# Performance work log

Hardware: AMD Instinct MI355X
Metric: run time of the kernel (lower is better)

Reference implementation:

```python
import jax, jax.numpy as jnp
import numpy as np

EMBED_DIM = 1024

def setup_inputs() -> dict:
    key = jax.random.key(0)
    kx, kq, kk, kv = jax.random.split(key, 4)
    scale = 1.0 / np.sqrt(EMBED_DIM)  # Kaiming-uniform-ish init scale
    x = jax.random.normal(kx, (4, 2048, EMBED_DIM), dtype=jnp.float32)
    Wq = jax.random.uniform(kq, (EMBED_DIM, EMBED_DIM), jnp.float32, -scale, scale)
    Wk = jax.random.uniform(kk, (EMBED_DIM, EMBED_DIM), jnp.float32, -scale, scale)
    Wv = jax.random.uniform(kv, (EMBED_DIM, EMBED_DIM), jnp.float32, -scale, scale)
    return {"x": x, "Wq": Wq, "Wk": Wk, "Wv": Wv}

def reference(x, Wq, Wk, Wv):
    # Linear layers: y = x @ W.T (torch nn.Linear convention, no bias)
    q = jnp.einsum('bsd,ed->bse', x, Wq)
    k = jnp.einsum('bsd,ed->bse', x, Wk)
    v = jnp.einsum('bsd,ed->bse', x, Wv)
    d = k.shape[-1]
    scores = jnp.einsum('bqe,bke->bqk', q, k) / jnp.sqrt(jnp.asarray(d, x.dtype))
    attn = jax.nn.softmax(scores, axis=-1)
    return jnp.einsum('bqk,bke->bqe', attn, v)
```

## Files before the change

### kernel.cpp

```cpp
#include <hip/hip_runtime.h>
#include <hip/hip_bf16.h>

typedef unsigned short u16;
typedef __bf16 bf16x8 __attribute__((ext_vector_type(8)));
typedef float f32x4 __attribute__((ext_vector_type(4)));

#define MEMF() asm volatile("" ::: "memory")

__device__ __forceinline__ u16 f2bf(float f) {
    unsigned int u = __builtin_bit_cast(unsigned int, f);
    unsigned int r = u + 0x7FFFu + ((u >> 16) & 1u);
    return (u16)(r >> 16);
}

__device__ __forceinline__ float bf2f(unsigned int bits16) {
    return __builtin_bit_cast(float, bits16 << 16);
}

__device__ __forceinline__ void gload_lds16(const u16* g, u16* l) {
    __builtin_amdgcn_global_load_lds(
        (const __attribute__((address_space(1))) void*)(g),
        (__attribute__((address_space(3))) void*)(l), 16, 0, 0);
}

__global__ __launch_bounds__(256) void cvt_bf16_kernel(
    const float* __restrict__ in, u16* __restrict__ out, int n8)
{
    int i = blockIdx.x * 256 + threadIdx.x;
    if (i >= n8) return;
    const float4* p = (const float4*)in + 2 * (long long)i;
    float4 a = p[0], b = p[1];
    uint4 o;
    o.x = (unsigned)f2bf(a.x) | ((unsigned)f2bf(a.y) << 16);
    o.y = (unsigned)f2bf(a.z) | ((unsigned)f2bf(a.w) << 16);
    o.z = (unsigned)f2bf(b.x) | ((unsigned)f2bf(b.y) << 16);
    o.w = (unsigned)f2bf(b.z) | ((unsigned)f2bf(b.w) << 16);
    ((uint4*)out)[i] = o;
}

template <int BN, bool OUT_F32>
__global__ __launch_bounds__(512, 2) void gemm4p(
    const u16* __restrict__ A, const u16* __restrict__ B, void* __restrict__ Cv,
    int lda, int ldb, int ldc, int K,
    long long sAz, long long sBz, long long sCz, int cw, int ch)
{
    constexpr int WC = (BN == 256) ? 4 : 2;
    constexpr int ROWS = (BN == 256) ? 128 : 64;
    constexpr int MI = ROWS / 16;
    constexpr int MIh = MI / 2;
    constexpr int BLOADS = BN / 64;
    constexpr int BNK = BN * 64;

    extern __shared__ u16 lds[];
    u16* ldsB = lds + 32768;

    const int flat = blockIdx.x + gridDim.x * blockIdx.y;
    const int xcd = flat & 7, jj = flat >> 3;
    const int nCx = gridDim.x / cw;
    const int bx = (xcd % nCx) * cw + jj % cw;
    const int by = (xcd / nCx) * ch + jj / cw;

    const int z = blockIdx.z;
    A += (long long)z * sAz;
    B += (long long)z * sBz;

    const int tid  = threadIdx.x;
    const int lane = tid & 63;
    const int wave = tid >> 6;
    const int wr = wave / WC, wc = wave % WC;
    const int m0 = by << 8, n0 = bx * BN;
    const int NT = K >> 6;

    const u16* gAp[4];
    const u16* gBp[BLOADS];
#pragma unroll
    for (int i = 0; i < 4; ++i) {
        int s = tid + i * 512, row = ((s >> 7) << 4) | (s & 15), g = (s >> 4) & 7;
        gAp[i] = A + (long long)(m0 + row) * lda + g * 8;
    }
#pragma unroll
    for (int i = 0; i < BLOADS; ++i) {
        int s = tid + i * 512, row = ((s >> 7) << 4) | (s & 15), g = (s >> 4) & 7;
        gBp[i] = B + (long long)(n0 + row) * ldb + g * 8;
    }
    auto stA = [&](int kt, int buf, int i) {
        gload_lds16(gAp[i] + (long long)kt * 64, lds + buf * 16384 + (tid + i * 512) * 8);
    };
    auto stB = [&](int kt, int buf, int i) {
        gload_lds16(gBp[i] + (long long)kt * 64, ldsB + buf * BNK + (tid + i * 512) * 8);
    };

    f32x4 acc[MI][4] = {};

#pragma unroll
    for (int i = 0; i < 4; ++i) stA(0, 0, i);
#pragma unroll
    for (int i = 0; i < BLOADS; ++i) stB(0, 0, i);
#pragma unroll
    for (int i = 0; i < 4; ++i) stA(1, 1, i);
#pragma unroll
    for (int i = 0; i < BLOADS; ++i) stB(1, 1, i);
    if constexpr (BN == 256) asm volatile("s_waitcnt vmcnt(8)" ::: "memory");
    else                     asm volatile("s_waitcnt vmcnt(6)" ::: "memory");
    __builtin_amdgcn_s_barrier();
    MEMF();

    for (int kt = 0; kt < NT; ++kt) {
        const int cur = kt & 1;
        const u16* sAc = lds  + cur * 16384 + lane * 8;
        const u16* sBc = ldsB + cur * BNK   + lane * 8;
        const bool st = (kt + 2 < NT);

        bf16x8 a[MIh][2], b0[2][2], b1[2][2];

#pragma unroll
        for (int mi = 0; mi < MIh; ++mi)
#pragma unroll
            for (int kk = 0; kk < 2; ++kk)
                a[mi][kk] = *(const bf16x8*)(sAc + ((wr * MI + mi) * 8 + kk * 4) * 128);
#pragma unroll
        for (int ni = 0; ni < 2; ++ni)
#pragma unroll
            for (int kk = 0; kk < 2; ++kk)
                b0[ni][kk] = *(const bf16x8*)(sBc + ((wc * 4 + ni) * 8 + kk * 4) * 128);
        MEMF(); __builtin_amdgcn_s_barrier();
        asm volatile("s_waitcnt lgkmcnt(0)" ::: "memory");
        __builtin_amdgcn_s_setprio(1);
#pragma unroll
        for (int kk = 0; kk < 2; ++kk)
#pragma unroll
            for (int mi = 0; mi < MIh; ++mi)
#pragma unroll
                for (int ni = 0; ni < 2; ++ni)
                    acc[mi][ni] = __builtin_amdgcn_mfma_f32_16x16x32_bf16(
                        a[mi][kk], b0[ni][kk], acc[mi][ni], 0, 0, 0);
        __builtin_amdgcn_s_setprio(0);
        MEMF(); __builtin_amdgcn_s_barrier();

#pragma unroll
        for (int ni = 0; ni < 2; ++ni)
#pragma unroll
            for (int kk = 0; kk < 2; ++kk)
                b1[ni][kk] = *(const bf16x8*)(sBc + ((wc * 4 + 2 + ni) * 8 + kk * 4) * 128);
        if constexpr (BN == 256) {
            if (st) { stA(kt + 2, cur, 0); stA(kt + 2, cur, 2); }
        }
        MEMF(); __builtin_amdgcn_s_barrier();
        asm volatile("s_waitcnt lgkmcnt(0)" ::: "memory");
        __builtin_amdgcn_s_setprio(1);
#pragma unroll
        for (int kk = 0; kk < 2; ++kk)
#pragma unroll
            for (int mi = 0; mi < MIh; ++mi)
#pragma unroll
                for (int ni = 0; ni < 2; ++ni)
                    acc[mi][2 + ni] = __builtin_amdgcn_mfma_f32_16x16x32_bf16(
                        a[mi][kk], b1[ni][kk], acc[mi][2 + ni], 0, 0, 0);
        __builtin_amdgcn_s_setprio(0);
        MEMF(); __builtin_amdgcn_s_barrier();

#pragma unroll
        for (int mi = 0; mi < MIh; ++mi)
#pragma unroll
            for (int kk = 0; kk < 2; ++kk)
                a[mi][kk] = *(const bf16x8*)(sAc + ((wr * MI + MIh + mi) * 8 + kk * 4) * 128);
        if (st) {
            if constexpr (BN == 256) { stB(kt + 2, cur, 0); stB(kt + 2, cur, 1); }
            else                     { stB(kt + 2, cur, 0); }
        }
        MEMF(); __builtin_amdgcn_s_barrier();
        asm volatile("s_waitcnt lgkmcnt(0)" ::: "memory");
        __builtin_amdgcn_s_setprio(1);
#pragma unroll
        for (int kk = 0; kk < 2; ++kk)
#pragma unroll
            for (int mi = 0; mi < MIh; ++mi)
#pragma unroll
                for (int ni = 0; ni < 2; ++ni)
                    acc[MIh + mi][ni] = __builtin_amdgcn_mfma_f32_16x16x32_bf16(
                        a[mi][kk], b0[ni][kk], acc[MIh + mi][ni], 0, 0, 0);
        __builtin_amdgcn_s_setprio(0);
        MEMF(); __builtin_amdgcn_s_barrier();

        if (st) {
            if constexpr (BN == 256) {
                stA(kt + 2, cur, 1); stA(kt + 2, cur, 3);
                stB(kt + 2, cur, 2); stB(kt + 2, cur, 3);
            } else {
                stA(kt + 2, cur, 0); stA(kt + 2, cur, 1);
                stA(kt + 2, cur, 2); stA(kt + 2, cur, 3);
                stB(kt + 2, cur, 1);
            }
        }
        MEMF(); __builtin_amdgcn_s_barrier();
        __builtin_amdgcn_s_setprio(1);
#pragma unroll
        for (int kk = 0; kk < 2; ++kk)
#pragma unroll
            for (int mi = 0; mi < MIh; ++mi)
#pragma unroll
                for (int ni = 0; ni < 2; ++ni)
                    acc[MIh + mi][2 + ni] = __builtin_amdgcn_mfma_f32_16x16x32_bf16(
                        a[mi][kk], b1[ni][kk], acc[MIh + mi][2 + ni], 0, 0, 0);
        __builtin_amdgcn_s_setprio(0);
        if (st) {
            if constexpr (BN == 256) asm volatile("s_waitcnt vmcnt(8)" ::: "memory");
            else                     asm volatile("s_waitcnt vmcnt(6)" ::: "memory");
        } else if (kt + 1 < NT) {
            asm volatile("s_waitcnt vmcnt(0)" ::: "memory");
        }
        MEMF(); __builtin_amdgcn_s_barrier();
    }

    const int fl = lane & 15, fg = lane >> 4;
    const int er0 = m0 + wr * ROWS + fg * 4;
    const int ec0 = n0 + wc * 64 + fl;
    if constexpr (OUT_F32) {
        float* C = (float*)Cv + (long long)z * sCz;
#pragma unroll
        for (int mi = 0; mi < MI; ++mi)
#pragma unroll
            for (int ni = 0; ni < 4; ++ni)
#pragma unroll
                for (int j = 0; j < 4; ++j)
                    C[(long long)(er0 + mi * 16 + j) * ldc + ec0 + ni * 16] = acc[mi][ni][j];
    } else {
        u16* C = (u16*)Cv + (long long)z * sCz;
#pragma unroll
        for (int mi = 0; mi < MI; ++mi)
#pragma unroll
            for (int ni = 0; ni < 4; ++ni)
#pragma unroll
                for (int j = 0; j < 4; ++j)
                    C[(long long)(er0 + mi * 16 + j) * ldc + ec0 + ni * 16] = f2bf(acc[mi][ni][j]);
    }
}

__global__ __launch_bounds__(256) void softmax_rows(u16* __restrict__ S)
{
    const long long row = blockIdx.x;
    u16* p = S + row * 2048;
    const int tid = threadIdx.x;
    const int lane = tid & 63, wave = tid >> 6;

    uint4 r4 = ((const uint4*)p)[tid];
    unsigned u[4] = {r4.x, r4.y, r4.z, r4.w};
    float v[8];
    const float scale = 1.0f / 32.0f;
#pragma unroll
    for (int i = 0; i < 4; ++i) {
        v[2 * i]     = bf2f(u[i] & 0xFFFFu) * scale;
        v[2 * i + 1] = __builtin_bit_cast(float, u[i] & 0xFFFF0000u) * scale;
    }
    float mx = v[0];
#pragma unroll
    for (int i = 1; i < 8; ++i) mx = fmaxf(mx, v[i]);
#pragma unroll
    for (int off = 32; off >= 1; off >>= 1) mx = fmaxf(mx, __shfl_xor(mx, off, 64));

    __shared__ float redmax[4], redsum[4];
    if (lane == 0) redmax[wave] = mx;
    __syncthreads();
    mx = fmaxf(fmaxf(redmax[0], redmax[1]), fmaxf(redmax[2], redmax[3]));

    float s = 0.f;
#pragma unroll
    for (int i = 0; i < 8; ++i) { v[i] = __expf(v[i] - mx); s += v[i]; }
#pragma unroll
    for (int off = 32; off >= 1; off >>= 1) s += __shfl_xor(s, off, 64);
    if (lane == 0) redsum[wave] = s;
    __syncthreads();
    s = redsum[0] + redsum[1] + redsum[2] + redsum[3];
    float inv = 1.0f / s;

    uint4 o;
    unsigned ov[4];
#pragma unroll
    for (int i = 0; i < 4; ++i)
        ov[i] = (unsigned)f2bf(v[2 * i] * inv) |
                ((unsigned)f2bf(v[2 * i + 1] * inv) << 16);
    o.x = ov[0]; o.y = ov[1]; o.z = ov[2]; o.w = ov[3];
    ((uint4*)p)[tid] = o;
}

extern "C" void kernel_launch(void* const* d_in, const int* in_sizes, int n_in,
                              void* d_out, int out_size, void* d_ws, size_t ws_size,
                              hipStream_t stream) {
    const float* x  = (const float*)d_in[0];
    const float* Wq = (const float*)d_in[1];
    const float* Wk = (const float*)d_in[2];
    const float* Wv = (const float*)d_in[3];
    float* out = (float*)d_out;

    const int B = 4, S = 2048, D = 1024;
    const long long MS = (long long)B * S;

    u16* Sc  = (u16*)d_ws;
    u16* xb  = Sc;
    u16* wqk = Sc  + (long long)B * S * S;
    u16* wvb = wqk + 2 * D * D;
    u16* qk  = wvb + D * D;
    u16* vT  = qk  + MS * 2 * D;
    size_t need = (size_t)2 * ((long long)B * S * S + 3 * D * D + MS * 2 * D + MS * D);
    if (ws_size < need) return;

    hipFuncSetAttribute(reinterpret_cast<const void*>(&gemm4p<256, false>),
                        hipFuncAttributeMaxDynamicSharedMemorySize, 131072);
    hipFuncSetAttribute(reinterpret_cast<const void*>(&gemm4p<128, false>),
                        hipFuncAttributeMaxDynamicSharedMemorySize, 98304);
    hipFuncSetAttribute(reinterpret_cast<const void*>(&gemm4p<128, true>),
                        hipFuncAttributeMaxDynamicSharedMemorySize, 98304);

    cvt_bf16_kernel<<<(int)(MS * D / 8 / 256), 256, 0, stream>>>(x, xb, (int)(MS * D / 8));
    cvt_bf16_kernel<<<D * D / 8 / 256, 256, 0, stream>>>(Wq, wqk, D * D / 8);
    cvt_bf16_kernel<<<D * D / 8 / 256, 256, 0, stream>>>(Wk, wqk + D * D, D * D / 8);
    cvt_bf16_kernel<<<D * D / 8 / 256, 256, 0, stream>>>(Wv, wvb, D * D / 8);

    gemm4p<256, false><<<dim3(2 * D / 256, (int)(MS / 256), 1), 512, 131072, stream>>>(
        xb, wqk, qk, D, D, 2 * D, D, 0, 0, 0, 8, 4);

    gemm4p<128, false><<<dim3((int)(MS / 128), D / 256, 1), 512, 98304, stream>>>(
        wvb, xb, vT, D, D, (int)MS, D, 0, 0, 0, 8, 4);

    gemm4p<256, false><<<dim3(S / 256, S / 256, B), 512, 131072, stream>>>(
        qk, qk + D, Sc, 2 * D, 2 * D, S, D,
        (long long)S * 2 * D, (long long)S * 2 * D, (long long)S * S, 2, 4);

    softmax_rows<<<(int)(B * S), 256, 0, stream>>>(Sc);

    gemm4p<128, true><<<dim3(D / 128, S / 256, B), 512, 98304, stream>>>(
        Sc, vT, out, S, (int)MS, D, S,
        (long long)S * S, (long long)S, (long long)S * D, 4, 2);
}
```

Baseline: 195.3 us.

## Double-buffer MFMA fragments in registers and prefetch next k-tile during compute

Restructures the GEMM main loop so the next k-tile's A and B fragments are read from LDS into separate register sets (a0/a1, b0/b1) while MFMAs for the current tile run. Global-to-LDS staging for tile kt+2 is now issued in one batch instead of being spread across the four phases. Explicit lgkmcnt waits are replaced by sched_barriers so LDS reads can overlap with matrix math. The cost is more registers and a full vmcnt(0) drain each iteration. There is also a possible race: the next buffer is read right after the wait with no barrier, so other waves' LDS writes may not be visible yet.

```diff
diff --git a/kernel.cpp b/kernel.cpp
--- a/kernel.cpp
+++ b/kernel.cpp
@@ -4,8 +4,6 @@
 typedef unsigned short u16;
 typedef __bf16 bf16x8 __attribute__((ext_vector_type(8)));
 typedef float f32x4 __attribute__((ext_vector_type(4)));
-
-#define MEMF() asm volatile("" ::: "memory")
 
 __device__ __forceinline__ u16 f2bf(float f) {
     unsigned int u = __builtin_bit_cast(unsigned int, f);
@@ -83,48 +81,48 @@
         int s = tid + i * 512, row = ((s >> 7) << 4) | (s & 15), g = (s >> 4) & 7;
         gBp[i] = B + (long long)(n0 + row) * ldb + g * 8;
     }
-    auto stA = [&](int kt, int buf, int i) {
-        gload_lds16(gAp[i] + (long long)kt * 64, lds + buf * 16384 + (tid + i * 512) * 8);
+    auto stage = [&](int kt, int buf) {
+#pragma unroll
+        for (int i = 0; i < 4; ++i)
+            gload_lds16(gAp[i] + (long long)kt * 64, lds + buf * 16384 + (tid + i * 512) * 8);
+#pragma unroll
+        for (int i = 0; i < BLOADS; ++i)
+            gload_lds16(gBp[i] + (long long)kt * 64, ldsB + buf * BNK + (tid + i * 512) * 8);
     };
-    auto stB = [&](int kt, int buf, int i) {
-        gload_lds16(gBp[i] + (long long)kt * 64, ldsB + buf * BNK + (tid + i * 512) * 8);
-    };
 
     f32x4 acc[MI][4] = {};
-
-#pragma unroll
-    for (int i = 0; i < 4; ++i) stA(0, 0, i);
-#pragma unroll
-    for (int i = 0; i < BLOADS; ++i) stB(0, 0, i);
-#pragma unroll
-    for (int i = 0; i < 4; ++i) stA(1, 1, i);
-#pragma unroll
-    for (int i = 0; i < BLOADS; ++i) stB(1, 1, i);
+    bf16x8 a0[MIh][2], a1[MIh][2], b0[2][2], b1[2][2];
+
+    stage(0, 0);
+    stage(1, 1);
     if constexpr (BN == 256) asm volatile("s_waitcnt vmcnt(8)" ::: "memory");
     else                     asm volatile("s_waitcnt vmcnt(6)" ::: "memory");
     __builtin_amdgcn_s_barrier();
-    MEMF();
+#pragma unroll
+    for (int mi = 0; mi < MIh; ++mi)
+#pragma unroll
+        for (int kk = 0; kk < 2; ++kk)
+            a0[mi][kk] = *(const bf16x8*)(lds + lane * 8 + ((wr * MI + mi) * 8 + kk * 4) * 128);
+#pragma unroll
+    for (int ni = 0; ni < 2; ++ni)
+#pragma unroll
+        for (int kk = 0; kk < 2; ++kk)
+            b0[ni][kk] = *(const bf16x8*)(ldsB + lane * 8 + ((wc * 4 + ni) * 8 + kk * 4) * 128);
 
     for (int kt = 0; kt < NT; ++kt) {
         const int cur = kt & 1;
         const u16* sAc = lds  + cur * 16384 + lane * 8;
         const u16* sBc = ldsB + cur * BNK   + lane * 8;
-        const bool st = (kt + 2 < NT);
-
-        bf16x8 a[MIh][2], b0[2][2], b1[2][2];
-
-#pragma unroll
-        for (int mi = 0; mi < MIh; ++mi)
+        const u16* sAn = lds  + (cur ^ 1) * 16384 + lane * 8;
+        const u16* sBn = ldsB + (cur ^ 1) * BNK   + lane * 8;
+
+#pragma unroll
+        for (int ni = 0; ni < 2; ++ni)
 #pragma unroll
             for (int kk = 0; kk < 2; ++kk)
-                a[mi][kk] = *(const bf16x8*)(sAc + ((wr * MI + mi) * 8 + kk * 4) * 128);
-#pragma unroll
-        for (int ni = 0; ni < 2; ++ni)
-#pragma unroll
-            for (int kk = 0; kk < 2; ++kk)
-                b0[ni][kk] = *(const bf16x8*)(sBc + ((wc * 4 + ni) * 8 + kk * 4) * 128);
-        MEMF(); __builtin_amdgcn_s_barrier();
-        asm volatile("s_waitcnt lgkmcnt(0)" ::: "memory");
+                b1[ni][kk] = *(const bf16x8*)(sBc + ((wc * 4 + 2 + ni) * 8 + kk * 4) * 128);
+        __builtin_amdgcn_sched_barrier(0);
+        __builtin_amdgcn_s_barrier();
         __builtin_amdgcn_s_setprio(1);
 #pragma unroll
         for (int kk = 0; kk < 2; ++kk)
@@ -133,20 +131,17 @@
 #pragma unroll
                 for (int ni = 0; ni < 2; ++ni)
                     acc[mi][ni] = __builtin_amdgcn_mfma_f32_16x16x32_bf16(
-                        a[mi][kk], b0[ni][kk], acc[mi][ni], 0, 0, 0);
+                        a0[mi][kk], b0[ni][kk], acc[mi][ni], 0, 0, 0);
         __builtin_amdgcn_s_setprio(0);
-        MEMF(); __builtin_amdgcn_s_barrier();
-
-#pragma unroll
-        for (int ni = 0; ni < 2; ++ni)
+        __builtin_amdgcn_s_barrier();
+
+#pragma unroll
+        for (int mi = 0; mi < MIh; ++mi)
 #pragma unroll
             for (int kk = 0; kk < 2; ++kk)
-                b1[ni][kk] = *(const bf16x8*)(sBc + ((wc * 4 + 2 + ni) * 8 + kk * 4) * 128);
-        if constexpr (BN == 256) {
-            if (st) { stA(kt + 2, cur, 0); stA(kt + 2, cur, 2); }
-        }
-        MEMF(); __builtin_amdgcn_s_barrier();
-        asm volatile("s_waitcnt lgkmcnt(0)" ::: "memory");
+                a1[mi][kk] = *(const bf16x8*)(sAc + ((wr * MI + MIh + mi) * 8 + kk * 4) * 128);
+        __builtin_amdgcn_sched_barrier(0);
+        __builtin_amdgcn_s_barrier();
         __builtin_amdgcn_s_setprio(1);
 #pragma unroll
         for (int kk = 0; kk < 2; ++kk)
@@ -155,21 +150,20 @@
 #pragma unroll
                 for (int ni = 0; ni < 2; ++ni)
                     acc[mi][2 + ni] = __builtin_amdgcn_mfma_f32_16x16x32_bf16(
-                        a[mi][kk], b1[ni][kk], acc[mi][2 + ni], 0, 0, 0);
+                        a0[mi][kk], b1[ni][kk], acc[mi][2 + ni], 0, 0, 0);
         __builtin_amdgcn_s_setprio(0);
-        MEMF(); __builtin_amdgcn_s_barrier();
-
-#pragma unroll
-        for (int mi = 0; mi < MIh; ++mi)
-#pragma unroll
-            for (int kk = 0; kk < 2; ++kk)
-                a[mi][kk] = *(const bf16x8*)(sAc + ((wr * MI + MIh + mi) * 8 + kk * 4) * 128);
-        if (st) {
-            if constexpr (BN == 256) { stB(kt + 2, cur, 0); stB(kt + 2, cur, 1); }
-            else                     { stB(kt + 2, cur, 0); }
+        __builtin_amdgcn_s_barrier();
+
+        if (kt + 1 < NT) {
+            asm volatile("s_waitcnt vmcnt(0)" ::: "memory");
+#pragma unroll
+            for (int mi = 0; mi < MIh; ++mi)
+#pragma unroll
+                for (int kk = 0; kk < 2; ++kk)
+                    a0[mi][kk] = *(const bf16x8*)(sAn + ((wr * MI + mi) * 8 + kk * 4) * 128);
         }
-        MEMF(); __builtin_amdgcn_s_barrier();
-        asm volatile("s_waitcnt lgkmcnt(0)" ::: "memory");
+        __builtin_amdgcn_sched_barrier(0);
+        __builtin_amdgcn_s_barrier();
         __builtin_amdgcn_s_setprio(1);
 #pragma unroll
         for (int kk = 0; kk < 2; ++kk)
@@ -178,21 +172,20 @@
 #pragma unroll
                 for (int ni = 0; ni < 2; ++ni)
                     acc[MIh + mi][ni] = __builtin_amdgcn_mfma_f32_16x16x32_bf16(
-                        a[mi][kk], b0[ni][kk], acc[MIh + mi][ni], 0, 0, 0);
+                        a1[mi][kk], b0[ni][kk], acc[MIh + mi][ni], 0, 0, 0);
         __builtin_amdgcn_s_setprio(0);
-        MEMF(); __builtin_amdgcn_s_barrier();
-
-        if (st) {
-            if constexpr (BN == 256) {
-                stA(kt + 2, cur, 1); stA(kt + 2, cur, 3);
-                stB(kt + 2, cur, 2); stB(kt + 2, cur, 3);
-            } else {
-                stA(kt + 2, cur, 0); stA(kt + 2, cur, 1);
-                stA(kt + 2, cur, 2); stA(kt + 2, cur, 3);
-                stB(kt + 2, cur, 1);
-            }
+        __builtin_amdgcn_s_barrier();
+
+        if (kt + 2 < NT) stage(kt + 2, cur);
+        if (kt + 1 < NT) {
+#pragma unroll
+            for (int ni = 0; ni < 2; ++ni)
+#pragma unroll
+                for (int kk = 0; kk < 2; ++kk)
+                    b0[ni][kk] = *(const bf16x8*)(sBn + ((wc * 4 + ni) * 8 + kk * 4) * 128);
         }
-        MEMF(); __builtin_amdgcn_s_barrier();
+        __builtin_amdgcn_sched_barrier(0);
+        __builtin_amdgcn_s_barrier();
         __builtin_amdgcn_s_setprio(1);
 #pragma unroll
         for (int kk = 0; kk < 2; ++kk)
@@ -201,15 +194,9 @@
 #pragma unroll
                 for (int ni = 0; ni < 2; ++ni)
                     acc[MIh + mi][2 + ni] = __builtin_amdgcn_mfma_f32_16x16x32_bf16(
-                        a[mi][kk], b1[ni][kk], acc[MIh + mi][2 + ni], 0, 0, 0);
+                        a1[mi][kk], b1[ni][kk], acc[MIh + mi][2 + ni], 0, 0, 0);
         __builtin_amdgcn_s_setprio(0);
-        if (st) {
-            if constexpr (BN == 256) asm volatile("s_waitcnt vmcnt(8)" ::: "memory");
-            else                     asm volatile("s_waitcnt vmcnt(6)" ::: "memory");
-        } else if (kt + 1 < NT) {
-            asm volatile("s_waitcnt vmcnt(0)" ::: "memory");
-        }
-        MEMF(); __builtin_amdgcn_s_barrier();
+        __builtin_amdgcn_s_barrier();
     }
 
     const int fl = lane & 15, fg = lane >> 4;
```

Measured after the change: 227.2 us. +16.3%, slower.

## Fuse softmax into QK^T epilogue and defer normalization to PV epilogue

Applied to the files above, without the earlier changes.

Removes the standalone softmax pass. The QK^T GEMM epilogue now writes exp(score/32) directly as bf16 and emits per-tile row-sum partials. A small kernel reduces those partials to inverse sums, and the PV GEMM scales its output rows by them. The three weight conversions are merged into one launch, and the compiler memory fences around barriers are dropped. The change skips max subtraction, which is safe for these input scales but could overflow for larger scores, and removing the fences risks compiler reordering of LDS accesses.

```diff
diff --git a/kernel.cpp b/kernel.cpp
--- a/kernel.cpp
+++ b/kernel.cpp
@@ -4,8 +4,6 @@
 typedef unsigned short u16;
 typedef __bf16 bf16x8 __attribute__((ext_vector_type(8)));
 typedef float f32x4 __attribute__((ext_vector_type(4)));
-
-#define MEMF() asm volatile("" ::: "memory")
 
 __device__ __forceinline__ u16 f2bf(float f) {
     unsigned int u = __builtin_bit_cast(unsigned int, f);
@@ -38,11 +36,41 @@
     ((uint4*)out)[i] = o;
 }
 
-template <int BN, bool OUT_F32>
+__global__ __launch_bounds__(256) void cvt3_bf16_kernel(
+    const float* __restrict__ a, const float* __restrict__ b,
+    const float* __restrict__ c, u16* __restrict__ out, int n8per)
+{
+    int i = blockIdx.x * 256 + threadIdx.x;
+    if (i >= n8per) return;
+    const float* in = (blockIdx.y == 0) ? a : ((blockIdx.y == 1) ? b : c);
+    const float4* p = (const float4*)in + 2 * (long long)i;
+    float4 va = p[0], vb = p[1];
+    uint4 o;
+    o.x = (unsigned)f2bf(va.x) | ((unsigned)f2bf(va.y) << 16);
+    o.y = (unsigned)f2bf(va.z) | ((unsigned)f2bf(va.w) << 16);
+    o.z = (unsigned)f2bf(vb.x) | ((unsigned)f2bf(vb.y) << 16);
+    o.w = (unsigned)f2bf(vb.z) | ((unsigned)f2bf(vb.w) << 16);
+    ((uint4*)(out + (long long)blockIdx.y * n8per * 8))[i] = o;
+}
+
+__global__ __launch_bounds__(256) void inv_rows(
+    const float* __restrict__ partial, float* __restrict__ inv, int n)
+{
+    int i = blockIdx.x * 256 + threadIdx.x;
+    if (i >= n) return;
+    const float* p = partial + (long long)i * 8;
+    float s = 0.f;
+#pragma unroll
+    for (int k = 0; k < 8; ++k) s += p[k];
+    inv[i] = 1.0f / s;
+}
+
+template <int BN, bool OUT_F32, int EPI>
 __global__ __launch_bounds__(512, 2) void gemm4p(
     const u16* __restrict__ A, const u16* __restrict__ B, void* __restrict__ Cv,
     int lda, int ldb, int ldc, int K,
-    long long sAz, long long sBz, long long sCz, int cw, int ch)
+    long long sAz, long long sBz, long long sCz, int cw, int ch,
+    float* __restrict__ aux)
 {
     constexpr int WC = (BN == 256) ? 4 : 2;
     constexpr int ROWS = (BN == 256) ? 128 : 64;
@@ -103,7 +131,6 @@
     if constexpr (BN == 256) asm volatile("s_waitcnt vmcnt(8)" ::: "memory");
     else                     asm volatile("s_waitcnt vmcnt(6)" ::: "memory");
     __builtin_amdgcn_s_barrier();
-    MEMF();
 
     for (int kt = 0; kt < NT; ++kt) {
         const int cur = kt & 1;
@@ -123,7 +150,7 @@
 #pragma unroll
             for (int kk = 0; kk < 2; ++kk)
                 b0[ni][kk] = *(const bf16x8*)(sBc + ((wc * 4 + ni) * 8 + kk * 4) * 128);
-        MEMF(); __builtin_amdgcn_s_barrier();
+        __builtin_amdgcn_s_barrier();
         asm volatile("s_waitcnt lgkmcnt(0)" ::: "memory");
         __builtin_amdgcn_s_setprio(1);
 #pragma unroll
@@ -135,7 +162,7 @@
                     acc[mi][ni] = __builtin_amdgcn_mfma_f32_16x16x32_bf16(
                         a[mi][kk], b0[ni][kk], acc[mi][ni], 0, 0, 0);
         __builtin_amdgcn_s_setprio(0);
-        MEMF(); __builtin_amdgcn_s_barrier();
+        __builtin_amdgcn_s_barrier();
 
 #pragma unroll
         for (int ni = 0; ni < 2; ++ni)
@@ -145,7 +172,7 @@
         if constexpr (BN == 256) {
             if (st) { stA(kt + 2, cur, 0); stA(kt + 2, cur, 2); }
         }
-        MEMF(); __builtin_amdgcn_s_barrier();
+        __builtin_amdgcn_s_barrier();
         asm volatile("s_waitcnt lgkmcnt(0)" ::: "memory");
         __builtin_amdgcn_s_setprio(1);
 #pragma unroll
@@ -157,7 +184,7 @@
                     acc[mi][2 + ni] = __builtin_amdgcn_mfma_f32_16x16x32_bf16(
                         a[mi][kk], b1[ni][kk], acc[mi][2 + ni], 0, 0, 0);
         __builtin_amdgcn_s_setprio(0);
-        MEMF(); __builtin_amdgcn_s_barrier();
+        __builtin_amdgcn_s_barrier();
 
 #pragma unroll
         for (int mi = 0; mi < MIh; ++mi)
@@ -168,7 +195,7 @@
             if constexpr (BN == 256) { stB(kt + 2, cur, 0); stB(kt + 2, cur, 1); }
             else                     { stB(kt + 2, cur, 0); }
         }
-        MEMF(); __builtin_amdgcn_s_barrier();
+        __builtin_amdgcn_s_barrier();
         asm volatile("s_waitcnt lgkmcnt(0)" ::: "memory");
         __builtin_amdgcn_s_setprio(1);
 #pragma unroll
@@ -180,7 +207,7 @@
                     acc[MIh + mi][ni] = __builtin_amdgcn_mfma_f32_16x16x32_bf16(
                         a[mi][kk], b0[ni][kk], acc[MIh + mi][ni], 0, 0, 0);
         __builtin_amdgcn_s_setprio(0);
-        MEMF(); __builtin_amdgcn_s_barrier();
+        __builtin_amdgcn_s_barrier();
 
         if (st) {
             if constexpr (BN == 256) {
@@ -192,7 +219,7 @@
                 stB(kt + 2, cur, 1);
             }
         }
-        MEMF(); __builtin_amdgcn_s_barrier();
+        __builtin_amdgcn_s_barrier();
         __builtin_amdgcn_s_setprio(1);
 #pragma unroll
         for (int kk = 0; kk < 2; ++kk)
@@ -209,13 +236,67 @@
         } else if (kt + 1 < NT) {
             asm volatile("s_waitcnt vmcnt(0)" ::: "memory");
         }
-        MEMF(); __builtin_amdgcn_s_barrier();
+        __builtin_amdgcn_s_barrier();
     }
 
     const int fl = lane & 15, fg = lane >> 4;
     const int er0 = m0 + wr * ROWS + fg * 4;
     const int ec0 = n0 + wc * 64 + fl;
-    if constexpr (OUT_F32) {
+
+    if constexpr (EPI == 1) {
+        u16* C = (u16*)Cv + (long long)z * sCz;
+        float lsum[MI][4];
+#pragma unroll
+        for (int mi = 0; mi < MI; ++mi)
+#pragma unroll
+            for (int j = 0; j < 4; ++j) {
+                float s = 0.f;
+#pragma unroll
+                for (int ni = 0; ni < 4; ++ni) {
+                    float e = __expf(acc[mi][ni][j] * 0.03125f);
+                    u16 h = f2bf(e);
+                    C[(long long)(er0 + mi * 16 + j) * ldc + ec0 + ni * 16] = h;
+                    s += bf2f(h);
+                }
+                lsum[mi][j] = s;
+            }
+#pragma unroll
+        for (int mi = 0; mi < MI; ++mi)
+#pragma unroll
+            for (int j = 0; j < 4; ++j)
+#pragma unroll
+                for (int off = 1; off < 16; off <<= 1)
+                    lsum[mi][j] += __shfl_xor(lsum[mi][j], off, 64);
+        float (*rsbuf)[4] = reinterpret_cast<float(*)[4]>(lds);
+        if (fl == 0) {
+#pragma unroll
+            for (int mi = 0; mi < MI; ++mi)
+#pragma unroll
+                for (int j = 0; j < 4; ++j)
+                    rsbuf[wr * ROWS + mi * 16 + fg * 4 + j][wc] = lsum[mi][j];
+        }
+        __syncthreads();
+        if (tid < 256) {
+            float s = rsbuf[tid][0] + rsbuf[tid][1] + rsbuf[tid][2] + rsbuf[tid][3];
+            aux[((long long)z * 2048 + m0 + tid) * 8 + bx] = s;
+        }
+    } else if constexpr (EPI == 2) {
+        float* C = (float*)Cv + (long long)z * sCz;
+        float iv[MI][4];
+#pragma unroll
+        for (int mi = 0; mi < MI; ++mi)
+#pragma unroll
+            for (int j = 0; j < 4; ++j)
+                iv[mi][j] = aux[(long long)z * 2048 + er0 + mi * 16 + j];
+#pragma unroll
+        for (int mi = 0; mi < MI; ++mi)
+#pragma unroll
+            for (int ni = 0; ni < 4; ++ni)
+#pragma unroll
+                for (int j = 0; j < 4; ++j)
+                    C[(long long)(er0 + mi * 16 + j) * ldc + ec0 + ni * 16] =
+                        acc[mi][ni][j] * iv[mi][j];
+    } else if constexpr (OUT_F32) {
         float* C = (float*)Cv + (long long)z * sCz;
 #pragma unroll
         for (int mi = 0; mi < MI; ++mi)
@@ -234,53 +315,6 @@
                 for (int j = 0; j < 4; ++j)
                     C[(long long)(er0 + mi * 16 + j) * ldc + ec0 + ni * 16] = f2bf(acc[mi][ni][j]);
     }
-}
-
-__global__ __launch_bounds__(256) void softmax_rows(u16* __restrict__ S)
-{
-    const long long row = blockIdx.x;
-    u16* p = S + row * 2048;
-    const int tid = threadIdx.x;
-    const int lane = tid & 63, wave = tid >> 6;
-
-    uint4 r4 = ((const uint4*)p)[tid];
-    unsigned u[4] = {r4.x, r4.y, r4.z, r4.w};
-    float v[8];
-    const float scale = 1.0f / 32.0f;
-#pragma unroll
-    for (int i = 0; i < 4; ++i) {
-        v[2 * i]     = bf2f(u[i] & 0xFFFFu) * scale;
-        v[2 * i + 1] = __builtin_bit_cast(float, u[i] & 0xFFFF0000u) * scale;
-    }
-    float mx = v[0];
-#pragma unroll
-    for (int i = 1; i < 8; ++i) mx = fmaxf(mx, v[i]);
-#pragma unroll
-    for (int off = 32; off >= 1; off >>= 1) mx = fmaxf(mx, __shfl_xor(mx, off, 64));
-
-    __shared__ float redmax[4], redsum[4];
-    if (lane == 0) redmax[wave] = mx;
-    __syncthreads();
-    mx = fmaxf(fmaxf(redmax[0], redmax[1]), fmaxf(redmax[2], redmax[3]));
-
-    float s = 0.f;
-#pragma unroll
-    for (int i = 0; i < 8; ++i) { v[i] = __expf(v[i] - mx); s += v[i]; }
-#pragma unroll
-    for (int off = 32; off >= 1; off >>= 1) s += __shfl_xor(s, off, 64);
-    if (lane == 0) redsum[wave] = s;
-    __syncthreads();
-    s = redsum[0] + redsum[1] + redsum[2] + redsum[3];
-    float inv = 1.0f / s;
-
-    uint4 o;
-    unsigned ov[4];
-#pragma unroll
-    for (int i = 0; i < 4; ++i)
-        ov[i] = (unsigned)f2bf(v[2 * i] * inv) |
-                ((unsigned)f2bf(v[2 * i + 1] * inv) << 16);
-    o.x = ov[0]; o.y = ov[1]; o.z = ov[2]; o.w = ov[3];
-    ((uint4*)p)[tid] = o;
 }
 
 extern "C" void kernel_launch(void* const* d_in, const int* in_sizes, int n_in,
@@ -301,34 +335,38 @@
     u16* wvb = wqk + 2 * D * D;
     u16* qk  = wvb + D * D;
     u16* vT  = qk  + MS * 2 * D;
-    size_t need = (size_t)2 * ((long long)B * S * S + 3 * D * D + MS * 2 * D + MS * D);
+    float* partial = (float*)(vT + MS * D);
+    float* inv     = partial + (long long)MS * 8;
+    size_t need = (size_t)2 * ((long long)B * S * S + 3 * D * D + MS * 2 * D + MS * D)
+                + (size_t)4 * (MS * 8 + MS);
     if (ws_size < need) return;
 
-    hipFuncSetAttribute(reinterpret_cast<const void*>(&gemm4p<256, false>),
+    hipFuncSetAttribute(reinterpret_cast<const void*>(&gemm4p<256, false, 0>),
                         hipFuncAttributeMaxDynamicSharedMemorySize, 131072);
-    hipFuncSetAttribute(reinterpret_cast<const void*>(&gemm4p<128, false>),
+    hipFuncSetAttribute(reinterpret_cast<const void*>(&gemm4p<128, false, 0>),
                         hipFuncAttributeMaxDynamicSharedMemorySize, 98304);
-    hipFuncSetAttribute(reinterpret_cast<const void*>(&gemm4p<128, true>),
+    hipFuncSetAttribute(reinterpret_cast<const void*>(&gemm4p<256, false, 1>),
+                        hipFuncAttributeMaxDynamicSharedMemorySize, 131072);
+    hipFuncSetAttribute(reinterpret_cast<const void*>(&gemm4p<128, true, 2>),
                         hipFuncAttributeMaxDynamicSharedMemorySize, 98304);
 
     cvt_bf16_kernel<<<(int)(MS * D / 8 / 256), 256, 0, stream>>>(x, xb, (int)(MS * D / 8));
-    cvt_bf16_kernel<<<D * D / 8 / 256, 256, 0, stream>>>(Wq, wqk, D * D / 8);
-    cvt_bf16_kernel<<<D * D / 8 / 256, 256, 0, stream>>>(Wk, wqk + D * D, D * D / 8);
-    cvt_bf16_kernel<<<D * D / 8 / 256, 256, 0, stream>>>(Wv, wvb, D * D / 8);
-
-    gemm4p<256, false><<<dim3(2 * D / 256, (int)(MS / 256), 1), 512, 131072, stream>>>(
-        xb, wqk, qk, D, D, 2 * D, D, 0, 0, 0, 8, 4);
-
-    gemm4p<128, false><<<dim3((int)(MS / 128), D / 256, 1), 512, 98304, stream>>>(
-        wvb, xb, vT, D, D, (int)MS, D, 0, 0, 0, 8, 4);
-
-    gemm4p<256, false><<<dim3(S / 256, S / 256, B), 512, 131072, stream>>>(
+    cvt3_bf16_kernel<<<dim3(D * D / 8 / 256, 3, 1), 256, 0, stream>>>(
+        Wq, Wk, Wv, wqk, D * D / 8);
+
+    gemm4p<256, false, 0><<<dim3(2 * D / 256, (int)(MS / 256), 1), 512, 131072, stream>>>(
+        xb, wqk, qk, D, D, 2 * D, D, 0, 0, 0, 8, 4, nullptr);
+
+    gemm4p<128, false, 0><<<dim3((int)(MS / 128), D / 256, 1), 512, 98304, stream>>>(
+        wvb, xb, vT, D, D, (int)MS, D, 0, 0, 0, 8, 4, nullptr);
+
+    gemm4p<256, false, 1><<<dim3(S / 256, S / 256, B), 512, 131072, stream>>>(
         qk, qk + D, Sc, 2 * D, 2 * D, S, D,
-        (long long)S * 2 * D, (long long)S * 2 * D, (long long)S * S, 2, 4);
-
-    softmax_rows<<<(int)(B * S), 256, 0, stream>>>(Sc);
-
-    gemm4p<128, true><<<dim3(D / 128, S / 256, B), 512, 98304, stream>>>(
+        (long long)S * 2 * D, (long long)S * 2 * D, (long long)S * S, 2, 4, partial);
+
+    inv_rows<<<(int)(MS / 256), 256, 0, stream>>>(partial, inv, (int)MS);
+
+    gemm4p<128, true, 2><<<dim3(D / 128, S / 256, B), 512, 98304, stream>>>(
         Sc, vT, out, S, (int)MS, D, S,
-        (long long)S * S, (long long)S, (long long)S * D, 4, 2);
-}
+        (long long)S * S, (long long)S, (long long)S * D, 4, 2, inv);
+}
```

Measured after the change: 182.7 us. 1.07x faster.
